# Kernel optimization log

Measured on AMD Instinct MI355X. Metric: run time of the kernel, lower is better.

## Reference

```python
import math
import jax, jax.numpy as jnp
import numpy as np


def setup_inputs() -> dict:
    key = jax.random.key(0)
    k1, k2, k3, k4 = jax.random.split(key, 4)
    B, K, D = 131072, 64, 8
    NC = D * (D + 1) // 2  # 36
    pi = jax.random.uniform(k1, (B, K), dtype=jnp.float32)
    mu = jax.random.normal(k2, (K, D), dtype=jnp.float32)
    # 'ALREADY CONSTRAINED' Cholesky entries: keep them positive (uniform),
    # +0.1 offset keeps diagonal safely away from 0 for the log.
    L_constrained = jax.random.uniform(k3, (K, NC), dtype=jnp.float32) + 0.1
    target = jax.random.normal(k4, (B, D), dtype=jnp.float32)
    return {"pi": pi, "mu": mu, "L_constrained": L_constrained, "target": target}


def reference(pi, mu, L_constrained, target):
    B, K = pi.shape
    D = mu.shape[1]
    norm_const = -0.5 * D * math.log(2.0 * math.pi)
    ti, tj = np.tril_indices(D)
    # scatter packed cholesky into dense lower-triangular (K, D, D)
    L = jnp.zeros((K, D, D), dtype=target.dtype).at[:, ti, tj].set(L_constrained)
    diff = target[:, None, :] - mu[None, :, :]          # (B, K, D)
    # batch over components, treat B as multiple RHS: L (K,D,D) @ z = b (K,D,B)
    b = jnp.transpose(diff, (1, 2, 0))                   # (K, D, B)
    z = jax.scipy.linalg.solve_triangular(L, b, lower=True)  # (K, D, B)
    M = jnp.sum(z * z, axis=1)                           # (K, B) Mahalanobis^2
    log_dets = jnp.sum(jnp.log(jnp.diagonal(L, axis1=-2, axis2=-1)), axis=-1)  # (K,)
    log_probs = norm_const - log_dets[:, None] - 0.5 * M  # (K, B)
    weighted = log_probs.T + jnp.log(pi + 1e-10)          # (B, K)
    nll = -jnp.mean(jax.scipy.special.logsumexp(weighted, axis=1))
    return nll
```

## Files before the change

kernel.cpp:

```cpp
#include <hip/hip_runtime.h>
#include <math.h>

#define B_TOTAL 131072
#define K_COMP  64
#define D_DIM   8
#define NC      36
#define NFEAT   96
#define ROWS_PB 256
#define RT_PW   4

#define NORM_CONST (-7.3515082656373815f)

typedef __attribute__((ext_vector_type(8))) short bf16x8;
typedef __attribute__((ext_vector_type(4))) float f32x4;

static __device__ __forceinline__ unsigned short bf16_rne(float x) {
    unsigned u = __float_as_uint(x);
    u += 0x7FFF + ((u >> 16) & 1);
    return (unsigned short)(u >> 16);
}
static __device__ __forceinline__ float bf16_f32(unsigned short h) {
    return __uint_as_float(((unsigned)h) << 16);
}

__global__ void mdn_precompute(const float* __restrict__ mu,
                               const float* __restrict__ Lc,
                               unsigned short* __restrict__ psi_hi,
                               unsigned short* __restrict__ psi_lo,
                               float* __restrict__ out) {
    int k = threadIdx.x;
    if (k == 0) out[0] = 0.0f;
    if (k >= K_COMP) return;
    const float* Lk = Lc + k * NC;

    float L[D_DIM][D_DIM];
    float W[D_DIM][D_DIM];
#pragma unroll
    for (int i = 0; i < D_DIM; i++)
#pragma unroll
        for (int j = 0; j < D_DIM; j++) { L[i][j] = 0.0f; W[i][j] = 0.0f; }

    float logdet = 0.0f;
    int idx = 0;
#pragma unroll
    for (int i = 0; i < D_DIM; i++)
#pragma unroll
        for (int j = 0; j <= i; j++) {
            float v = Lk[idx++];
            L[i][j] = v;
            if (j == i) logdet += logf(v);
        }

#pragma unroll
    for (int j = 0; j < D_DIM; j++) {
        W[j][j] = 1.0f / L[j][j];
#pragma unroll
        for (int i = 0; i < D_DIM; i++) {
            if (i > j) {
                float acc = 0.0f;
#pragma unroll
                for (int m = 0; m < D_DIM; m++)
                    if (m >= j && m < i) acc += L[i][m] * W[m][j];
                W[i][j] = -acc / L[i][i];
            }
        }
    }

    float P[D_DIM][D_DIM];
#pragma unroll
    for (int a = 0; a < D_DIM; a++)
#pragma unroll
        for (int b = 0; b < D_DIM; b++) {
            float acc = 0.0f;
#pragma unroll
            for (int m = 0; m < D_DIM; m++) acc += W[m][a] * W[m][b];
            P[a][b] = acc;
        }

    float h[D_DIM];
    float qf = 0.0f;
#pragma unroll
    for (int i = 0; i < D_DIM; i++) {
        float acc = 0.0f;
#pragma unroll
        for (int j = 0; j < D_DIM; j++) acc += P[i][j] * mu[k * D_DIM + j];
        h[i] = acc;
        qf += mu[k * D_DIM + i] * acc;
    }
    float g = NORM_CONST - logdet - 0.5f * qf;

    float psi[NFEAT];
#pragma unroll
    for (int e = 0; e < NFEAT; e++) psi[e] = 0.0f;
#pragma unroll
    for (int a = 0; a < D_DIM; a++)
#pragma unroll
        for (int b = 0; b < D_DIM; b++) psi[8 * a + b] = -0.5f * P[a][b];
#pragma unroll
    for (int b = 0; b < D_DIM; b++) psi[64 + b] = h[b];
    psi[72] = g;

    unsigned short* oh = psi_hi + k * NFEAT;
    unsigned short* ol = psi_lo + k * NFEAT;
#pragma unroll
    for (int e = 0; e < NFEAT; e++) {
        unsigned short hi = bf16_rne(psi[e]);
        oh[e] = hi;
        ol[e] = bf16_rne(psi[e] - bf16_f32(hi));
    }
}

__global__ __launch_bounds__(256, 2) void mdn_main(
        const float* __restrict__ pi,
        const unsigned short* __restrict__ psi_hi,
        const unsigned short* __restrict__ psi_lo,
        const float* __restrict__ target,
        float* __restrict__ out) {
    const int tid = threadIdx.x;
    const int lane = tid & 63;
    const int w = tid >> 6;
    const int q = lane >> 4;
    const int n = lane & 15;
    const int rowbase = blockIdx.x * ROWS_PB;

    __shared__ float Tl[ROWS_PB * D_DIM];
    {
        const float4* src = (const float4*)(target + (size_t)rowbase * D_DIM);
        float4* dst = (float4*)Tl;
        dst[tid] = src[tid];
        dst[tid + 256] = src[tid + 256];
    }

    bf16x8 Ah[4][3], Al[4][3];
#pragma unroll
    for (int mt = 0; mt < 4; mt++)
#pragma unroll
        for (int ks = 0; ks < 3; ks++) {
            const int off = (16 * mt + n) * NFEAT + 32 * ks + 8 * q;
            Ah[mt][ks] = *(const bf16x8*)(psi_hi + off);
            Al[mt][ks] = *(const bf16x8*)(psi_lo + off);
        }

    __syncthreads();

    float lacc = 0.0f;

#pragma unroll 2
    for (int r = 0; r < RT_PW; r++) {
        const int row0 = w * (RT_PW * 16) + r * 16;
        const int grow = rowbase + row0 + n;

        f32x4 pv4[4];
#pragma unroll
        for (int mt = 0; mt < 4; mt++)
            pv4[mt] = *(const f32x4*)(pi + (size_t)grow * K_COMP + 16 * mt + 4 * q);

        const f32x4* trow = (const f32x4*)(Tl + (row0 + n) * D_DIM);
        f32x4 tlo = trow[0], thi = trow[1];
        float tv[D_DIM] = {tlo[0], tlo[1], tlo[2], tlo[3],
                           thi[0], thi[1], thi[2], thi[3]};

        float ta0 = (q & 2) ? ((q & 1) ? tlo[3] : tlo[2]) : ((q & 1) ? tlo[1] : tlo[0]);
        float ta1 = (q & 2) ? ((q & 1) ? thi[3] : thi[2]) : ((q & 1) ? thi[1] : thi[0]);

        bf16x8 Bh[3], Bl[3];
#pragma unroll
        for (int j = 0; j < D_DIM; j++) {
            float f0 = ta0 * tv[j];
            unsigned short h0 = bf16_rne(f0);
            Bh[0][j] = (short)h0;
            Bl[0][j] = (short)bf16_rne(f0 - bf16_f32(h0));

            float f1 = ta1 * tv[j];
            unsigned short h1 = bf16_rne(f1);
            Bh[1][j] = (short)h1;
            Bl[1][j] = (short)bf16_rne(f1 - bf16_f32(h1));

            float f2 = (q == 0) ? tv[j] : ((q == 1 && j == 0) ? 1.0f : 0.0f);
            unsigned short h2 = bf16_rne(f2);
            Bh[2][j] = (short)h2;
            Bl[2][j] = (short)bf16_rne(f2 - bf16_f32(h2));
        }

        f32x4 acc[4];
#pragma unroll
        for (int mt = 0; mt < 4; mt++) {
            f32x4 a = {0.0f, 0.0f, 0.0f, 0.0f};
#pragma unroll
            for (int ks = 0; ks < 3; ks++) {
                a = __builtin_amdgcn_mfma_f32_16x16x32_bf16(Ah[mt][ks], Bh[ks], a, 0, 0, 0);
                a = __builtin_amdgcn_mfma_f32_16x16x32_bf16(Al[mt][ks], Bh[ks], a, 0, 0, 0);
                a = __builtin_amdgcn_mfma_f32_16x16x32_bf16(Ah[mt][ks], Bl[ks], a, 0, 0, 0);
            }
            acc[mt] = a;
        }

        float m0 = fmaxf(fmaxf(acc[0][0], acc[0][1]), fmaxf(acc[0][2], acc[0][3]));
        float m1 = fmaxf(fmaxf(acc[1][0], acc[1][1]), fmaxf(acc[1][2], acc[1][3]));
        float m2 = fmaxf(fmaxf(acc[2][0], acc[2][1]), fmaxf(acc[2][2], acc[2][3]));
        float m3 = fmaxf(fmaxf(acc[3][0], acc[3][1]), fmaxf(acc[3][2], acc[3][3]));
        float mrow = fmaxf(fmaxf(m0, m1), fmaxf(m2, m3));
        mrow = fmaxf(mrow, __shfl_xor(mrow, 16));
        mrow = fmaxf(mrow, __shfl_xor(mrow, 32));

        float s = 0.0f;
#pragma unroll
        for (int mt = 0; mt < 4; mt++) {
            s += (pv4[mt][0] + 1e-10f) * __expf(acc[mt][0] - mrow);
            s += (pv4[mt][1] + 1e-10f) * __expf(acc[mt][1] - mrow);
            s += (pv4[mt][2] + 1e-10f) * __expf(acc[mt][2] - mrow);
            s += (pv4[mt][3] + 1e-10f) * __expf(acc[mt][3] - mrow);
        }
        s += __shfl_xor(s, 16);
        s += __shfl_xor(s, 32);

        if (q == 0) lacc += mrow + __logf(s);
    }

#pragma unroll
    for (int off = 32; off > 0; off >>= 1) lacc += __shfl_down(lacc, off);
    __shared__ float wsum[4];
    if (lane == 0) wsum[w] = lacc;
    __syncthreads();
    if (tid == 0) {
        atomicAdd(out, (wsum[0] + wsum[1] + wsum[2] + wsum[3]) * (-1.0f / (float)B_TOTAL));
    }
}

extern "C" void kernel_launch(void* const* d_in, const int* in_sizes, int n_in,
                              void* d_out, int out_size, void* d_ws, size_t ws_size,
                              hipStream_t stream) {
    const float* pi  = (const float*)d_in[0];
    const float* mu  = (const float*)d_in[1];
    const float* Lc  = (const float*)d_in[2];
    const float* tgt = (const float*)d_in[3];
    float* out = (float*)d_out;

    unsigned short* psi_hi = (unsigned short*)d_ws;
    unsigned short* psi_lo = (unsigned short*)((char*)d_ws + K_COMP * NFEAT * 2);

    mdn_precompute<<<1, 64, 0, stream>>>(mu, Lc, psi_hi, psi_lo, out);
    mdn_main<<<B_TOTAL / ROWS_PB, 256, 0, stream>>>(pi, psi_hi, psi_lo, tgt, out);
}
```

Baseline: 93.54 us.

## Fuse per-component precompute into main kernel with LDS-staged coefficients

Removes the single-block precompute kernel and has each block of the main kernel redo the per-component Cholesky inversion and psi construction in its first wave, storing hi/lo bf16 coefficients in padded shared memory. The output zeroing moves to a hipMemsetAsync. This removes the serialized tiny launch and the global round trip, but adds redundant per-block serial work (one wave of 64 threads doing an 8x8 inverse) before the MFMA loop, plus more LDS use that may affect occupancy.

```diff
diff --git a/kernel.cpp b/kernel.cpp
--- a/kernel.cpp
+++ b/kernel.cpp
@@ -6,6 +6,7 @@
 #define D_DIM   8
 #define NC      36
 #define NFEAT   96
+#define NFP     104
 #define ROWS_PB 256
 #define RT_PW   4
 
@@ -23,97 +24,10 @@
     return __uint_as_float(((unsigned)h) << 16);
 }
 
-__global__ void mdn_precompute(const float* __restrict__ mu,
-                               const float* __restrict__ Lc,
-                               unsigned short* __restrict__ psi_hi,
-                               unsigned short* __restrict__ psi_lo,
-                               float* __restrict__ out) {
-    int k = threadIdx.x;
-    if (k == 0) out[0] = 0.0f;
-    if (k >= K_COMP) return;
-    const float* Lk = Lc + k * NC;
-
-    float L[D_DIM][D_DIM];
-    float W[D_DIM][D_DIM];
-#pragma unroll
-    for (int i = 0; i < D_DIM; i++)
-#pragma unroll
-        for (int j = 0; j < D_DIM; j++) { L[i][j] = 0.0f; W[i][j] = 0.0f; }
-
-    float logdet = 0.0f;
-    int idx = 0;
-#pragma unroll
-    for (int i = 0; i < D_DIM; i++)
-#pragma unroll
-        for (int j = 0; j <= i; j++) {
-            float v = Lk[idx++];
-            L[i][j] = v;
-            if (j == i) logdet += logf(v);
-        }
-
-#pragma unroll
-    for (int j = 0; j < D_DIM; j++) {
-        W[j][j] = 1.0f / L[j][j];
-#pragma unroll
-        for (int i = 0; i < D_DIM; i++) {
-            if (i > j) {
-                float acc = 0.0f;
-#pragma unroll
-                for (int m = 0; m < D_DIM; m++)
-                    if (m >= j && m < i) acc += L[i][m] * W[m][j];
-                W[i][j] = -acc / L[i][i];
-            }
-        }
-    }
-
-    float P[D_DIM][D_DIM];
-#pragma unroll
-    for (int a = 0; a < D_DIM; a++)
-#pragma unroll
-        for (int b = 0; b < D_DIM; b++) {
-            float acc = 0.0f;
-#pragma unroll
-            for (int m = 0; m < D_DIM; m++) acc += W[m][a] * W[m][b];
-            P[a][b] = acc;
-        }
-
-    float h[D_DIM];
-    float qf = 0.0f;
-#pragma unroll
-    for (int i = 0; i < D_DIM; i++) {
-        float acc = 0.0f;
-#pragma unroll
-        for (int j = 0; j < D_DIM; j++) acc += P[i][j] * mu[k * D_DIM + j];
-        h[i] = acc;
-        qf += mu[k * D_DIM + i] * acc;
-    }
-    float g = NORM_CONST - logdet - 0.5f * qf;
-
-    float psi[NFEAT];
-#pragma unroll
-    for (int e = 0; e < NFEAT; e++) psi[e] = 0.0f;
-#pragma unroll
-    for (int a = 0; a < D_DIM; a++)
-#pragma unroll
-        for (int b = 0; b < D_DIM; b++) psi[8 * a + b] = -0.5f * P[a][b];
-#pragma unroll
-    for (int b = 0; b < D_DIM; b++) psi[64 + b] = h[b];
-    psi[72] = g;
-
-    unsigned short* oh = psi_hi + k * NFEAT;
-    unsigned short* ol = psi_lo + k * NFEAT;
-#pragma unroll
-    for (int e = 0; e < NFEAT; e++) {
-        unsigned short hi = bf16_rne(psi[e]);
-        oh[e] = hi;
-        ol[e] = bf16_rne(psi[e] - bf16_f32(hi));
-    }
-}
-
-__global__ __launch_bounds__(256, 2) void mdn_main(
+__global__ __launch_bounds__(256, 2) void mdn_fused(
         const float* __restrict__ pi,
-        const unsigned short* __restrict__ psi_hi,
-        const unsigned short* __restrict__ psi_lo,
+        const float* __restrict__ mu,
+        const float* __restrict__ Lc,
         const float* __restrict__ target,
         float* __restrict__ out) {
     const int tid = threadIdx.x;
@@ -123,7 +37,10 @@
     const int n = lane & 15;
     const int rowbase = blockIdx.x * ROWS_PB;
 
+    __shared__ alignas(16) unsigned short psiH[K_COMP * NFP];
+    __shared__ alignas(16) unsigned short psiL[K_COMP * NFP];
     __shared__ float Tl[ROWS_PB * D_DIM];
+
     {
         const float4* src = (const float4*)(target + (size_t)rowbase * D_DIM);
         float4* dst = (float4*)Tl;
@@ -131,17 +48,98 @@
         dst[tid + 256] = src[tid + 256];
     }
 
+    if (tid < K_COMP) {
+        const int k = tid;
+        const float* Lk = Lc + k * NC;
+
+        float L[D_DIM][D_DIM];
+        float W[D_DIM][D_DIM];
+#pragma unroll
+        for (int i = 0; i < D_DIM; i++)
+#pragma unroll
+            for (int j = 0; j < D_DIM; j++) { L[i][j] = 0.0f; W[i][j] = 0.0f; }
+
+        float logdet = 0.0f;
+        int idx = 0;
+#pragma unroll
+        for (int i = 0; i < D_DIM; i++)
+#pragma unroll
+            for (int j = 0; j <= i; j++) {
+                float v = Lk[idx++];
+                L[i][j] = v;
+                if (j == i) logdet += logf(v);
+            }
+
+#pragma unroll
+        for (int j = 0; j < D_DIM; j++) {
+            W[j][j] = 1.0f / L[j][j];
+#pragma unroll
+            for (int i = 0; i < D_DIM; i++) {
+                if (i > j) {
+                    float acc = 0.0f;
+#pragma unroll
+                    for (int m = 0; m < D_DIM; m++)
+                        if (m >= j && m < i) acc += L[i][m] * W[m][j];
+                    W[i][j] = -acc / L[i][i];
+                }
+            }
+        }
+
+        float P[D_DIM][D_DIM];
+#pragma unroll
+        for (int a = 0; a < D_DIM; a++)
+#pragma unroll
+            for (int b = 0; b < D_DIM; b++) {
+                float acc = 0.0f;
+#pragma unroll
+                for (int m = 0; m < D_DIM; m++) acc += W[m][a] * W[m][b];
+                P[a][b] = acc;
+            }
+
+        float h[D_DIM];
+        float qf = 0.0f;
+#pragma unroll
+        for (int i = 0; i < D_DIM; i++) {
+            float acc = 0.0f;
+#pragma unroll
+            for (int j = 0; j < D_DIM; j++) acc += P[i][j] * mu[k * D_DIM + j];
+            h[i] = acc;
+            qf += mu[k * D_DIM + i] * acc;
+        }
+        float g = NORM_CONST - logdet - 0.5f * qf;
+
+        float psi[NFEAT];
+#pragma unroll
+        for (int e = 0; e < NFEAT; e++) psi[e] = 0.0f;
+#pragma unroll
+        for (int a = 0; a < D_DIM; a++)
+#pragma unroll
+            for (int b = 0; b < D_DIM; b++) psi[8 * a + b] = -0.5f * P[a][b];
+#pragma unroll
+        for (int b = 0; b < D_DIM; b++) psi[64 + b] = h[b];
+        psi[72] = g;
+
+        unsigned short* oh = psiH + k * NFP;
+        unsigned short* ol = psiL + k * NFP;
+#pragma unroll
+        for (int e = 0; e < NFEAT; e++) {
+            unsigned short hi = bf16_rne(psi[e]);
+            oh[e] = hi;
+            ol[e] = bf16_rne(psi[e] - bf16_f32(hi));
+        }
+    }
+
+    __syncthreads();
+
     bf16x8 Ah[4][3], Al[4][3];
 #pragma unroll
     for (int mt = 0; mt < 4; mt++)
 #pragma unroll
         for (int ks = 0; ks < 3; ks++) {
-            const int off = (16 * mt + n) * NFEAT + 32 * ks + 8 * q;
-            Ah[mt][ks] = *(const bf16x8*)(psi_hi + off);
-            Al[mt][ks] = *(const bf16x8*)(psi_lo + off);
-        }
-
-    __syncthreads();
+            const int off = (16 * mt + n) * NFP + 32 * ks + 8 * q;
+            Ah[mt][ks] = *(const bf16x8*)(psiH + off);
+            Al[mt][ks] = *(const bf16x8*)(psiL + off);
+        }
 
     float lacc = 0.0f;
 
@@ -236,9 +234,6 @@
     const float* tgt = (const float*)d_in[3];
     float* out = (float*)d_out;
 
-    unsigned short* psi_hi = (unsigned short*)d_ws;
-    unsigned short* psi_lo = (unsigned short*)((char*)d_ws + K_COMP * NFEAT * 2);
-
-    mdn_precompute<<<1, 64, 0, stream>>>(mu, Lc, psi_hi, psi_lo, out);
-    mdn_main<<<B_TOTAL / ROWS_PB, 256, 0, stream>>>(pi, psi_hi, psi_lo, tgt, out);
-}
+    hipMemsetAsync(out, 0, sizeof(float), stream);
+    mdn_fused<<<B_TOTAL / ROWS_PB, 256, 0, stream>>>(pi, mu, Lc, tgt, out);
+}
```

Result: faster. 91.57 us (-2.1%).
